# Performance work log

Measured on AMD Instinct MI355X. Metric: run time of the kernel, lower is better.

The kernel has to match this reference:

```python
import jax, jax.numpy as jnp
import numpy as np
import math

B, N, HORIZON, E = 16, 4096, 12, 16
IN_DIM = HORIZON * E            # 192
T_DIM, H, D = 64, 4, 16         # transformer_dim, heads, head_dim
K_ORD = 3
FFN = 128
OUT_DIM = HORIZON * 16          # horizon * dim_out = 192
LN_EPS = 1e-5


def setup_inputs() -> dict:
    key = jax.random.key(0)
    ks = jax.random.split(key, 16)
    s = 0.02
    return {
        "x": jax.random.normal(ks[0], (B, N, IN_DIM), jnp.float32),
        "Wq": jax.random.normal(ks[1], (IN_DIM, T_DIM), jnp.float32) * s,
        "bq": jnp.zeros((T_DIM,), jnp.float32),
        "Wk": jax.random.normal(ks[2], (IN_DIM, T_DIM), jnp.float32) * s,
        "bk": jnp.zeros((T_DIM,), jnp.float32),
        "Wv": jax.random.normal(ks[3], (IN_DIM, T_DIM), jnp.float32) * s,
        "bv": jnp.zeros((T_DIM,), jnp.float32),
        "Win": jax.random.normal(ks[4], (IN_DIM, T_DIM), jnp.float32) * s,  # no bias
        "Wout": jax.random.normal(ks[5], (T_DIM, OUT_DIM), jnp.float32) * s,
        "bout": jnp.zeros((OUT_DIM,), jnp.float32),
        "W1": jax.random.normal(ks[6], (T_DIM, FFN), jnp.float32) * s,
        "b1": jnp.zeros((FFN,), jnp.float32),
        "W2": jax.random.normal(ks[7], (FFN, T_DIM), jnp.float32) * s,
        "b2": jnp.zeros((T_DIM,), jnp.float32),
        "ln_g": jnp.ones((T_DIM,), jnp.float32),
        "ln_b": jnp.zeros((T_DIM,), jnp.float32),
        "weights_pool": jax.random.normal(ks[8], (IN_DIM, OUT_DIM), jnp.float32) * s,
        "Pi": jax.random.normal(ks[9], (H, K_ORD + 1), jnp.float32) * 0.5,
    }


def _layer_norm(y, g, b):
    mu = jnp.mean(y, axis=-1, keepdims=True)
    var = jnp.mean((y - mu) ** 2, axis=-1, keepdims=True)
    return (y - mu) * jax.lax.rsqrt(var + LN_EPS) * g + b


def reference(x, Wq, bq, Wk, bk, Wv, bv, Win, Wout, bout,
              W1, b1, W2, b2, ln_g, ln_b, weights_pool, Pi):
    Bx, Nx, _ = x.shape
    # projections -> (B, H, N, d)
    Q = (x @ Wq + bq).reshape(Bx, Nx, H, D).transpose(0, 2, 1, 3)
    Kt = (x @ Wk + bk).reshape(Bx, Nx, H, D).transpose(0, 2, 1, 3)
    V = (x @ Wv + bv).reshape(Bx, Nx, H, D).transpose(0, 2, 1, 3)

    weighted_sum = jnp.zeros((Bx, H, Nx, D), x.dtype)
    for k in range(K_ORD + 1):
        if k == 0:
            # transform(0, .) returns ones with feature dim 1
            Qk = jnp.ones((Bx, H, Nx, 1), x.dtype)
            Kk = jnp.ones((Bx, H, Nx, 1), x.dtype)
        else:
            Qk = Q ** k   # elementwise power (exp-by-squaring == x**k)
            Kk = Kt ** k
        dk = Qk.shape[-1]
        # f_kv: (B,H,f,d) ; sumN: (B,H,f,1)
        f_kv = jnp.einsum('bhnf,bhnc->bhfc', Kk, V)
        sumN = jnp.sum(Kk, axis=2)[..., None]
        f_kv_norm = f_kv / (sumN + 1e-8) / math.sqrt(dk)
        c_k = jnp.einsum('bhnf,bhfc->bhnc', Qk, f_kv_norm)
        weighted_sum = weighted_sum + c_k * Pi[:, k][None, :, None, None]

    # NOTE: faithful to original: raw view of (B,H,N,d) as (B,N,H*d), no permute
    attention_out = weighted_sum.reshape(Bx, Nx, H * D) / math.factorial(K_ORD)

    proj = x @ Win
    res = _layer_norm(proj + attention_out, ln_g, ln_b)
    ffn = jax.nn.relu(res @ W1 + b1) @ W2 + b2   # dropout = identity (eval)
    res = _layer_norm(res + ffn, ln_g, ln_b)

    x_g = jnp.einsum('bni,io->bno', x, weights_pool)
    out = res @ Wout + bout
    return x_g + out
```

## Files before the change

kernel.cpp:

```cpp
#include <hip/hip_runtime.h>

typedef unsigned int u32;
typedef unsigned short u16;

#define NB 16
#define NN 4096
#define IND 192

typedef __attribute__((ext_vector_type(8))) short short8;
typedef __attribute__((ext_vector_type(4))) float f32x4;
#define MFMA16 __builtin_amdgcn_mfma_f32_16x16x32_bf16

__device__ __forceinline__ float bf2f(u16 u) {
  union { u32 i; float f; } c; c.i = ((u32)u) << 16; return c.f;
}
__device__ __forceinline__ float lo16(u32 u) {
  union { u32 i; float f; } c; c.i = u << 16; return c.f;
}
__device__ __forceinline__ float hi16(u32 u) {
  union { u32 i; float f; } c; c.i = u & 0xffff0000u; return c.f;
}
__device__ __forceinline__ u16 f2bf(float f) {
  union { float f; u32 i; } c; c.f = f;
  u32 r = c.i + 0x7fffu + ((c.i >> 16) & 1u);
  return (u16)(r >> 16);
}
__device__ __forceinline__ float ldwf(const void* p, int i, int isf) {
  return isf ? ((const float*)p)[i] : bf2f(((const u16*)p)[i]);
}
__device__ __forceinline__ short8 ld_frag8(const u16* p) {
  union { uint4 u; short8 s; } c;
  c.u = *reinterpret_cast<const uint4*>(p);
  return c.s;
}
__device__ __forceinline__ short8 as_short8(uint4 u) {
  union { uint4 u; short8 s; } c; c.u = u; return c.s;
}
__device__ __forceinline__ short8 pack8(const float* v) {
  short8 s;
  #pragma unroll
  for (int e = 0; e < 8; ++e) s[e] = (short)f2bf(v[e]);
  return s;
}
__device__ __forceinline__ short8 packf4(float4 a, float4 b) {
  short8 s;
  s[0] = (short)f2bf(a.x); s[1] = (short)f2bf(a.y);
  s[2] = (short)f2bf(a.z); s[3] = (short)f2bf(a.w);
  s[4] = (short)f2bf(b.x); s[5] = (short)f2bf(b.y);
  s[6] = (short)f2bf(b.z); s[7] = (short)f2bf(b.w);
  return s;
}
__device__ __forceinline__ float ln64(float y, float g, float be) {
  float s = y, sq = y * y;
  #pragma unroll
  for (int off = 32; off > 0; off >>= 1) {
    s  += __shfl_xor(s, off, 64);
    sq += __shfl_xor(sq, off, 64);
  }
  float mu  = s * 0.015625f;
  float var = sq * 0.015625f - mu * mu;
  return (y - mu) * rsqrtf(var + 1e-5f) * g + be;
}

__global__ __launch_bounds__(64) void k_detect(const u32* __restrict__ x2,
                                               int* __restrict__ flag) {
  int t = threadIdx.x;
  int bad = 0;
  for (int i = 0; i < 16; ++i) {
    float a = fabsf(lo16(x2[t * 16 + i]));
    if (!(a < 1e4f)) bad = 1;
  }
  int anybad = __any(bad);
  if (t == 0) *flag = anybad ? 1 : 0;
}

__global__ __launch_bounds__(192) void k_xsum(const int* __restrict__ flag,
                                              const void* __restrict__ x,
                                              float* __restrict__ xsum) {
  const int isf = *flag;
  const int t = threadIdx.x;
  const int r0 = blockIdx.x * 256;
  const int b = r0 >> 12;
  float s = 0.f;
  if (isf) {
    const float* xp = (const float*)x;
    for (int r = 0; r < 256; ++r) s += xp[(size_t)(r0 + r) * 192 + t];
  } else {
    const u16* xp = (const u16*)x;
    for (int r = 0; r < 256; ++r) s += bf2f(xp[(size_t)(r0 + r) * 192 + t]);
  }
  atomicAdd(xsum + b * 192 + t, s);
}

__global__ __launch_bounds__(256) void k_prepw(
    const int* __restrict__ flag,
    const void* Wq, const void* Wk, const void* Wv, const void* Win,
    const void* Wout, const void* Wp, const void* W1, const void* W2,
    const void* bq, const void* bk, const void* bv,
    u16* __restrict__ Bs1, u16* __restrict__ BsKlo, u16* __restrict__ Bs2,
    u16* __restrict__ W1f, u16* __restrict__ W2f, float* __restrict__ bcat)
{
  const int isf = *flag;
  int idx = blockIdx.x * 256 + threadIdx.x;
  if (idx < 49152) {
    int e = idx & 7, l = (idx >> 3) & 63, g = idx >> 9;
    int nt = g & 15, ks = g >> 4;
    int k = ks * 32 + (l >> 4) * 8 + e;
    int n = nt * 16 + (l & 15);
    const void* W = (n < 64) ? Wq : (n < 128) ? Wk : (n < 192) ? Wv : Win;
    Bs1[idx] = f2bf(ldwf(W, k * 64 + (n & 63), isf));
  } else if (idx < 61440) {
    int j = idx - 49152;
    int e = j & 7, l = (j >> 3) & 63, g = j >> 9;
    int ntp = g & 3, ks = g >> 2;
    int k = ks * 32 + (l >> 4) * 8 + e;
    int n = ntp * 16 + (l & 15);
    float wv = ldwf(Wk, k * 64 + n, isf);
    u16 hi = f2bf(wv);
    BsKlo[j] = f2bf(wv - bf2f(hi));
  } else if (idx < 110592) {
    int j = idx - 61440;
    int e = j & 7, l = (j >> 3) & 63, g = j >> 9;
    int nt = g % 12, ks = g / 12;
    int k = ks * 32 + (l >> 4) * 8 + e;
    int n = nt * 16 + (l & 15);
    float v = (k < 64) ? ldwf(Wout, k * 192 + n, isf)
                       : ldwf(Wp, (k - 64) * 192 + n, isf);
    Bs2[j] = f2bf(v);
  } else if (idx < 118784) {
    int j = idx - 110592;
    int e = j & 7, l = (j >> 3) & 63, g = j >> 9;
    int nt = g & 7, ks = g >> 3;
    int k = ks * 32 + (l >> 4) * 8 + e;
    int n = nt * 16 + (l & 15);
    W1f[j] = f2bf(ldwf(W1, k * 128 + n, isf));
  } else if (idx < 126976) {
    int j = idx - 118784;
    int e = j & 7, l = (j >> 3) & 63, g = j >> 9;
    int nt = g & 3, ks = g >> 2;
    int k = ks * 32 + (l >> 4) * 8 + e;
    int n = nt * 16 + (l & 15);
    W2f[j] = f2bf(ldwf(W2, k * 64 + n, isf));
  } else if (idx < 127232) {
    int n = idx - 126976;
    bcat[n] = (n < 64)  ? ldwf(bq, n, isf)
            : (n < 128) ? ldwf(bk, n - 64, isf)
            : (n < 192) ? ldwf(bv, n - 128, isf) : 0.f;
  }
}

template<bool F32>
__device__ void gemm1_body(const void* __restrict__ x,
                           const u16* __restrict__ Bs1,
                           const u16* __restrict__ BsKlo,
                           const float* __restrict__ bcat,
                           u16* __restrict__ C1, float* __restrict__ stats,
                           float (*xs)[196], float (*Ks)[65], float (*Vs)[65])
{
  const int tid = threadIdx.x;
  const int mbase = blockIdx.x * 32;
  const int b = mbase >> 12;

  if constexpr (F32) {
    for (int i = tid; i < 1536; i += 512) {
      int row = i / 48, c4 = i - row * 48;
      float4 v = *((const float4*)x + (size_t)(mbase + row) * 48 + c4);
      *(float4*)&xs[row][c4 * 4] = v;
    }
    __syncthreads();
  }

  const int w = tid >> 6, l = tid & 63, lm = l & 15, lk = l >> 4;
  const int nt0 = w * 2;
  const bool isK = (w == 2) || (w == 3);

  short8 bhi[2][6], blo[2][6];
  #pragma unroll
  for (int n2 = 0; n2 < 2; ++n2)
    #pragma unroll
    for (int ks = 0; ks < 6; ++ks) {
      bhi[n2][ks] = ld_frag8(Bs1 + (size_t)((ks * 16 + nt0 + n2) * 64 + l) * 8);
      if (F32 && isK)
        blo[n2][ks] = ld_frag8(BsKlo + (size_t)((ks * 4 + nt0 + n2 - 4) * 64 + l) * 8);
    }
  float bias[2];
  bias[0] = bcat[nt0 * 16 + lm];
  bias[1] = bcat[(nt0 + 1) * 16 + lm];

  for (int mt = 0; mt < 2; ++mt) {
    short8 ahi[6], alo[6];
    if constexpr (F32) {
      const float* xr = &xs[mt * 16 + lm][0];
      #pragma unroll
      for (int ks = 0; ks < 6; ++ks) {
        float v[8];
        *(float4*)&v[0] = *(const float4*)(xr + ks * 32 + lk * 8);
        *(float4*)&v[4] = *(const float4*)(xr + ks * 32 + lk * 8 + 4);
        short8 h8;
        #pragma unroll
        for (int e = 0; e < 8; ++e) h8[e] = (short)f2bf(v[e]);
        ahi[ks] = h8;
        if (isK) {
          short8 l8;
          #pragma unroll
          for (int e = 0; e < 8; ++e) {
            float r = v[e] - bf2f((u16)h8[e]);
            l8[e] = (short)f2bf(r);
          }
          alo[ks] = l8;
        }
      }
    } else {
      const u16* xg = (const u16*)x + (size_t)(mbase + mt * 16 + lm) * 192 + lk * 8;
      #pragma unroll
      for (int ks = 0; ks < 6; ++ks) ahi[ks] = ld_frag8(xg + ks * 32);
    }
    f32x4 acc[2];
    #pragma unroll
    for (int n2 = 0; n2 < 2; ++n2) {
      f32x4 a = {bias[n2], bias[n2], bias[n2], bias[n2]};
      acc[n2] = a;
    }
    #pragma unroll
    for (int ks = 0; ks < 6; ++ks)
      #pragma unroll
      for (int n2 = 0; n2 < 2; ++n2) {
        acc[n2] = MFMA16(ahi[ks], bhi[n2][ks], acc[n2], 0, 0, 0);
        if (F32 && isK) {
          acc[n2] = MFMA16(ahi[ks], blo[n2][ks], acc[n2], 0, 0, 0);
          acc[n2] = MFMA16(alo[ks], bhi[n2][ks], acc[n2], 0, 0, 0);
          acc[n2] = MFMA16(alo[ks], blo[n2][ks], acc[n2], 0, 0, 0);
        }
      }
    const int rl = mt * 16 + lk * 4;
    if (w < 2) {
      #pragma unroll
      for (int n2 = 0; n2 < 2; ++n2)
        #pragma unroll
        for (int r = 0; r < 4; ++r)
          C1[(size_t)(mbase + rl + r) * 128 + (nt0 + n2) * 16 + lm] = f2bf(acc[n2][r]);
    } else if (isK) {
      #pragma unroll
      for (int n2 = 0; n2 < 2; ++n2)
        #pragma unroll
        for (int r = 0; r < 4; ++r)
          Ks[rl + r][(nt0 + n2 - 4) * 16 + lm] = acc[n2][r];
    } else if (w < 6) {
      #pragma unroll
      for (int n2 = 0; n2 < 2; ++n2)
        #pragma unroll
        for (int r = 0; r < 4; ++r)
          Vs[rl + r][(nt0 + n2 - 8) * 16 + lm] = acc[n2][r];
    } else {
      #pragma unroll
      for (int n2 = 0; n2 < 2; ++n2)
        #pragma unroll
        for (int r = 0; r < 4; ++r)
          C1[(size_t)(mbase + rl + r) * 128 + 64 + (nt0 + n2 - 12) * 16 + lm] = f2bf(acc[n2][r]);
    }
  }
  __syncthreads();

  float* sb = stats + (size_t)(b * 4) * 832;
  #pragma unroll
  for (int it = 0; it < 2; ++it) {
    int item = tid + it * 512;
    int hh = item >> 8, f = (item >> 4) & 15, c = item & 15;
    float a1 = 0.f, a2 = 0.f, a3 = 0.f;
    for (int r = 0; r < 32; ++r) {
      float kv = Ks[r][hh * 16 + f];
      float vv = Vs[r][hh * 16 + c];
      float k2 = kv * kv;
      a1 = fmaf(kv, vv, a1);
      a2 = fmaf(k2, vv, a2);
      a3 = fmaf(k2 * kv, vv, a3);
    }
    float* base = sb + (size_t)hh * 832 + f * 16 + c;
    atomicAdd(base, a1);
    atomicAdd(base + 256, a2);
    atomicAdd(base + 512, a3);
  }
  if (tid < 192) {
    int kk = tid >> 6, hf = tid & 63, h2 = hf >> 4, ff = hf & 15;
    float s = 0.f;
    for (int r = 0; r < 32; ++r) {
      float kv = Ks[r][hf];
      s += (kk == 0) ? kv : (kk == 1) ? kv * kv : kv * kv * kv;
    }
    atomicAdd(sb + (size_t)h2 * 832 + 768 + kk * 16 + ff, s);
  } else if (tid < 256) {
    int hf = tid - 192, h2 = hf >> 4;
    float s = 0.f;
    for (int r = 0; r < 32; ++r) s += Vs[r][hf];
    atomicAdd(sb + (size_t)h2 * 832 + 816 + (hf & 15), s);
  }
}

__global__ __launch_bounds__(512, 2) void k_gemm1(
    const int* __restrict__ flag, const void* __restrict__ x,
    const u16* __restrict__ Bs1, const u16* __restrict__ BsKlo,
    const float* __restrict__ bcat,
    u16* __restrict__ C1, float* __restrict__ stats)
{
  __shared__ float xs[32][196];
  __shared__ float Ks[32][65];
  __shared__ float Vs[32][65];
  if (*flag) gemm1_body<true >(x, Bs1, BsKlo, bcat, C1, stats, xs, Ks, Vs);
  else       gemm1_body<false>(x, Bs1, BsKlo, bcat, C1, stats, xs, Ks, Vs);
}

template<bool F32>
__device__ void finalize_body(const float* stats, const void* Pi,
                              const void* Wk, const void* bk,
                              const float* xsum, float* M, float* sn1)
{
  const int bh = blockIdx.x, bb = bh >> 2, h = bh & 3, t = threadIdx.x;
  const float* sb = stats + (size_t)bh * 832;
  float* mb = M + (size_t)bh * 784;
  const float inv6 = 1.0f / 6.0f;

  {
    int f = t >> 4, s = t & 15;
    float p = 0.f;
    for (int i = s * 12; i < s * 12 + 12; ++i)
      p += xsum[bb * 192 + i] * ldwf(Wk, i * 64 + h * 16 + f, F32);
    p += __shfl_xor(p, 1, 64);
    p += __shfl_xor(p, 2, 64);
    p += __shfl_xor(p, 4, 64);
    p += __shfl_xor(p, 8, 64);
    if (s == 0) sn1[f] = p + 4096.0f * ldwf(bk, h * 16 + f, F32);
  }
  __syncthreads();

  {
    const int f = t >> 4, c = t & 15;
    #pragma unroll
    for (int k = 0; k < 3; ++k) {
      float fkv = sb[k * 256 + f * 16 + c];
      float sk  = (k == 0) ? sn1[f] : sb[768 + k * 16 + f];
      float pi  = ldwf(Pi, h * 4 + (k + 1), F32);
      mb[k * 256 + f * 16 + c] = fkv / ((sk + 1e-8f) * 4.0f) * pi * inv6;
    }
  }
  if (t < 16) {
    float sv  = sb[816 + t];
    float pi0 = ldwf(Pi, h * 4 + 0, F32);
    mb[768 + t] = sv / (4096.0f + 1e-8f) * pi0 * inv6;
  }
}

__global__ __launch_bounds__(256) void k_finalize(
    const int* __restrict__ flag, const float* __restrict__ stats,
    const void* __restrict__ Pi, const void* __restrict__ Wk,
    const void* __restrict__ bk, const float* __restrict__ xsum,
    float* __restrict__ M)
{
  __shared__ float sn1[16];
  if (*flag) finalize_body<true >(stats, Pi, Wk, bk, xsum, M, sn1);
  else       finalize_body<false>(stats, Pi, Wk, bk, xsum, M, sn1);
}

template<bool F32> __device__ void mid_body(
    const u16* __restrict__ C1, u16* __restrict__ R2,
    const float* __restrict__ Mall,
    const u16* __restrict__ W1f, const u16* __restrict__ W2f,
    const void* __restrict__ b1, const void* __restrict__ b2,
    const void* __restrict__ lng, const void* __restrict__ lnb,
    float (*attL)[72], u16 (*resB)[72], u16 (*hB)[136])
{
  const int tid = threadIdx.x;
  const int w = tid >> 6, l = tid & 63;
  const int lm = l & 15, lk = l >> 4;
  const int n0g = blockIdx.x * 64;
  const int b = n0g >> 12;
  const int n2_0 = n0g & 4095;
  const int h = n2_0 >> 10;
  const int qg0 = (b << 12) + ((n2_0 & 1023) << 2);
  const float* mb = Mall + (size_t)((b << 2) + h) * 784;

  short8 Bhi[2], Blo[2];
  #pragma unroll
  for (int ks = 0; ks < 2; ++ks) {
    float vh[8], vl[8];
    #pragma unroll
    for (int e = 0; e < 8; ++e) {
      int kk = ks * 32 + lk * 8 + e;
      float v = (kk < 16) ? mb[kk * 16 + lm]
              : (kk < 32) ? mb[256 + (kk - 16) * 16 + lm]
              : (kk < 48) ? mb[512 + (kk - 32) * 16 + lm] : 0.f;
      float hi = bf2f(f2bf(v));
      vh[e] = hi; vl[e] = v - hi;
    }
    Bhi[ks] = pack8(vh);
    Blo[ks] = pack8(vl);
  }
  const float c0v = mb[768 + lm];

  #pragma unroll
  for (int mt2 = 0; mt2 < 4; ++mt2) {
    const int mt = w * 4 + mt2;
    uint4 qv = *(const uint4*)(C1 + (size_t)(qg0 + mt * 16 + lm) * 128
                               + h * 16 + (lk & 1) * 8);
    float q[8] = {lo16(qv.x), hi16(qv.x), lo16(qv.y), hi16(qv.y),
                  lo16(qv.z), hi16(qv.z), lo16(qv.w), hi16(qv.w)};
    float q2[8], q3[8];
    #pragma unroll
    for (int e = 0; e < 8; ++e) { q2[e] = q[e] * q[e]; q3[e] = q2[e] * q[e]; }
    short8 a1, a2;
    if (lk < 2) { a1 = as_short8(qv); a2 = pack8(q3); }
    else        { a1 = pack8(q2);     a2 = short8{0,0,0,0,0,0,0,0}; }

    f32x4 acc = {c0v, c0v, c0v, c0v};
    acc = MFMA16(a1, Bhi[0], acc, 0, 0, 0);
    acc = MFMA16(a1, Blo[0], acc, 0, 0, 0);
    acc = MFMA16(a2, Bhi[1], acc, 0, 0, 0);
    acc = MFMA16(a2, Blo[1], acc, 0, 0, 0);

    #pragma unroll
    for (int r = 0; r < 4; ++r) {
      int qr = mt * 16 + lk * 4 + r;
      attL[qr >> 2][(qr & 3) * 16 + lm] = acc[r];
    }
  }

  const float gj = ldwf(lng, l, F32), bj = ldwf(lnb, l, F32);
  #pragma unroll 4
  for (int rr = 0; rr < 16; ++rr) {
    int r = w * 16 + rr;
    float proj = bf2f(C1[(size_t)(n0g + r) * 128 + 64 + l]);
    float y = proj + attL[r][l];
    resB[r][l] = f2bf(ln64(y, gj, bj));
  }

  short8 a0 = *(const short8*)&resB[w * 16 + lm][lk * 8];
  short8 a1f = *(const short8*)&resB[w * 16 + lm][32 + lk * 8];
  f32x4 hacc[8];
  #pragma unroll
  for (int nt = 0; nt < 8; ++nt) {
    float bv = ldwf(b1, nt * 16 + lm, F32);
    f32x4 a = {bv, bv, bv, bv};
    hacc[nt] = a;
  }
  #pragma unroll
  for (int nt = 0; nt < 8; ++nt) {
    short8 w1a = ld_frag8(W1f + (size_t)((0 * 8 + nt) * 64 + l) * 8);
    short8 w1b = ld_frag8(W1f + (size_t)((1 * 8 + nt) * 64 + l) * 8);
    hacc[nt] = MFMA16(a0, w1a, hacc[nt], 0, 0, 0);
    hacc[nt] = MFMA16(a1f, w1b, hacc[nt], 0, 0, 0);
  }
  #pragma unroll
  for (int nt = 0; nt < 8; ++nt)
    #pragma unroll
    for (int r = 0; r < 4; ++r) {
      int row = w * 16 + lk * 4 + r;
      hB[row][nt * 16 + lm] = f2bf(fmaxf(hacc[nt][r], 0.f));
    }

  short8 ha[4];
  #pragma unroll
  for (int ks = 0; ks < 4; ++ks)
    ha[ks] = *(const short8*)&hB[w * 16 + lm][ks * 32 + lk * 8];
  f32x4 oacc[4];
  #pragma unroll
  for (int nt = 0; nt < 4; ++nt) {
    float bv = ldwf(b2, nt * 16 + lm, F32);
    f32x4 a = {bv, bv, bv, bv};
    oacc[nt] = a;
  }
  #pragma unroll
  for (int ks = 0; ks < 4; ++ks)
    #pragma unroll
    for (int nt = 0; nt < 4; ++nt) {
      short8 w2v = ld_frag8(W2f + (size_t)((ks * 4 + nt) * 64 + l) * 8);
      oacc[nt] = MFMA16(ha[ks], w2v, oacc[nt], 0, 0, 0);
    }

  float gcol[4], bcol[4];
  #pragma unroll
  for (int nt = 0; nt < 4; ++nt) {
    gcol[nt] = ldwf(lng, nt * 16 + lm, F32);
    bcol[nt] = ldwf(lnb, nt * 16 + lm, F32);
  }
  #pragma unroll
  for (int r = 0; r < 4; ++r) {
    int row = w * 16 + lk * 4 + r;
    float y[4];
    float s = 0.f, sq = 0.f;
    #pragma unroll
    for (int nt = 0; nt < 4; ++nt) {
      y[nt] = oacc[nt][r] + bf2f(resB[row][nt * 16 + lm]);
      s += y[nt];
      sq = fmaf(y[nt], y[nt], sq);
    }
    #pragma unroll
    for (int off = 8; off > 0; off >>= 1) {
      s  += __shfl_xor(s, off, 64);
      sq += __shfl_xor(sq, off, 64);
    }
    float mu = s * 0.015625f;
    float var = sq * 0.015625f - mu * mu;
    float rs = rsqrtf(var + 1e-5f);
    #pragma unroll
    for (int nt = 0; nt < 4; ++nt) {
      float r2v = (y[nt] - mu) * rs * gcol[nt] + bcol[nt];
      R2[(size_t)(n0g + row) * 64 + nt * 16 + lm] = f2bf(r2v);
    }
  }
}

__global__ __launch_bounds__(256, 2) void k_mid(
    const int* __restrict__ flag, const u16* __restrict__ C1,
    u16* __restrict__ R2, const float* __restrict__ Mall,
    const u16* __restrict__ W1f, const u16* __restrict__ W2f,
    const void* __restrict__ b1, const void* __restrict__ b2,
    const void* __restrict__ lng, const void* __restrict__ lnb)
{
  __shared__ float attL[64][72];
  __shared__ u16 resB[64][72];
  __shared__ u16 hB[64][136];
  if (*flag) mid_body<true >(C1, R2, Mall, W1f, W2f, b1, b2, lng, lnb, attL, resB, hB);
  else       mid_body<false>(C1, R2, Mall, W1f, W2f, b1, b2, lng, lnb, attL, resB, hB);
}

template<bool F32>
__device__ void gemm2_body(const void* __restrict__ x,
                           const u16* __restrict__ R2,
                           const u16* __restrict__ Bs2,
                           const void* __restrict__ bout,
                           void* __restrict__ out)
{
  const int l = threadIdx.x & 63;
  const int w = threadIdx.x >> 6;
  const int mbase = blockIdx.x * 64;
  const int lm = l & 15, lk = l >> 4;

  short8 bf[8][3];
  #pragma unroll
  for (int ks = 0; ks < 8; ++ks)
    #pragma unroll
    for (int nt = 0; nt < 3; ++nt)
      bf[ks][nt] = ld_frag8(Bs2 + (size_t)((ks * 12 + w * 3 + nt) * 64 + l) * 8);

  float bias[3];
  #pragma unroll
  for (int nt = 0; nt < 3; ++nt) bias[nt] = ldwf(bout, w * 48 + nt * 16 + lm, F32);

  for (int mt = 0; mt < 4; ++mt) {
    const int row = mbase + mt * 16 + lm;
    short8 af[8];
    {
      const u16* rp = R2 + (size_t)row * 64 + lk * 8;
      af[0] = ld_frag8(rp);
      af[1] = ld_frag8(rp + 32);
    }
    if constexpr (F32) {
      const float* xp = (const float*)x + (size_t)row * 192 + lk * 8;
      #pragma unroll
      for (int ks = 2; ks < 8; ++ks) {
        float4 va = *(const float4*)(xp + (ks - 2) * 32);
        float4 vb = *(const float4*)(xp + (ks - 2) * 32 + 4);
        af[ks] = packf4(va, vb);
      }
    } else {
      const u16* xp = (const u16*)x + (size_t)row * 192 + lk * 8;
      #pragma unroll
      for (int ks = 2; ks < 8; ++ks) af[ks] = ld_frag8(xp + (ks - 2) * 32);
    }

    f32x4 acc[3];
    #pragma unroll
    for (int nt = 0; nt < 3; ++nt) {
      f32x4 a = {bias[nt], bias[nt], bias[nt], bias[nt]};
      acc[nt] = a;
    }
    #pragma unroll
    for (int ks = 0; ks < 8; ++ks)
      #pragma unroll
      for (int nt = 0; nt < 3; ++nt)
        acc[nt] = MFMA16(af[ks], bf[ks][nt], acc[nt], 0, 0, 0);
    const int r0 = mbase + mt * 16 + lk * 4;
    const int c0 = w * 48 + lm;
    if constexpr (F32) {
      float* op = (float*)out;
      #pragma unroll
      for (int nt = 0; nt < 3; ++nt)
        #pragma unroll
        for (int r = 0; r < 4; ++r)
          op[(size_t)(r0 + r) * IND + c0 + nt * 16] = acc[nt][r];
    } else {
      u16* op = (u16*)out;
      #pragma unroll
      for (int nt = 0; nt < 3; ++nt)
        #pragma unroll
        for (int r = 0; r < 4; ++r)
          op[(size_t)(r0 + r) * IND + c0 + nt * 16] = f2bf(acc[nt][r]);
    }
  }
}

__global__ __launch_bounds__(256, 2) void k_gemm2(
    const int* __restrict__ flag, const void* __restrict__ x,
    const u16* __restrict__ R2, const u16* __restrict__ Bs2,
    const void* __restrict__ bout, void* __restrict__ out)
{
  if (*flag) gemm2_body<true >(x, R2, Bs2, bout, out);
  else       gemm2_body<false>(x, R2, Bs2, bout, out);
}

extern "C" void kernel_launch(void* const* d_in, const int* in_sizes, int n_in,
                              void* d_out, int out_size, void* d_ws, size_t ws_size,
                              hipStream_t stream)
{
  const void* x   = d_in[0];
  const void* Wq  = d_in[1];
  const void* bq  = d_in[2];
  const void* Wk  = d_in[3];
  const void* bk  = d_in[4];
  const void* Wv  = d_in[5];
  const void* bv  = d_in[6];
  const void* Win = d_in[7];
  const void* Wout= d_in[8];
  const void* bout= d_in[9];
  const void* W1  = d_in[10];
  const void* b1  = d_in[11];
  const void* W2  = d_in[12];
  const void* b2  = d_in[13];
  const void* lng = d_in[14];
  const void* lnb = d_in[15];
  const void* Wp  = d_in[16];
  const void* Pi  = d_in[17];

  u16* xb    = (u16*)d_ws;
  u16* C1    = xb + (size_t)12582912;
  u16* R2    = C1 + (size_t)8388608;
  u16* Bs1   = R2 + (size_t)4194304;
  u16* BsKlo = Bs1 + 49152;
  u16* Bs2   = BsKlo + 12288;
  u16* W1f   = Bs2 + 49152;
  u16* W2f   = W1f + 8192;
  float* bcat  = (float*)(W2f + 8192);
  float* stats = bcat + 256;
  float* xsum  = stats + 53248;
  float* Mc    = xsum + 3072;
  int*   flag  = (int*)(Mc + 50176);

  k_detect<<<1, 64, 0, stream>>>((const u32*)x, flag);
  hipMemsetAsync(stats, 0, (size_t)(53248 + 3072) * sizeof(float), stream);

  k_prepw<<<497, 256, 0, stream>>>(flag, Wq, Wk, Wv, Win, Wout, Wp, W1, W2,
                                   bq, bk, bv, Bs1, BsKlo, Bs2, W1f, W2f, bcat);
  k_xsum<<<256, 192, 0, stream>>>(flag, x, xsum);
  k_gemm1<<<2048, 512, 0, stream>>>(flag, x, Bs1, BsKlo, bcat, C1, stats);
  k_finalize<<<64, 256, 0, stream>>>(flag, stats, Pi, Wk, bk, xsum, Mc);
  k_mid<<<1024, 256, 0, stream>>>(flag, C1, R2, Mc, W1f, W2f, b1, b2, lng, lnb);
  k_gemm2<<<1024, 256, 0, stream>>>(flag, x, R2, Bs2, bout, d_out);
}
```

Baseline: 159.2 us.

## Split Q/Win GEMM from K/V stats kernel and replace atomics with partial-sum buffers

The fused projection+statistics kernel is split in two. A lean k_gemm1 computes only the Q and Win columns into C1, reading x directly from global memory. A new k_stats kernel recomputes the K and V projections over 128-row chunks, accumulates moment statistics in registers, and writes per-slice partials instead of issuing atomicAdds. k_finalize now reduces the 32 partial slices. This aims to remove atomic contention and the shared-memory staging of x, at the cost of reading x twice and a larger partials workspace.

Result: slower. 214.5 us (+34.7%).

```diff
diff --git a/kernel.cpp b/kernel.cpp
--- a/kernel.cpp
+++ b/kernel.cpp
@@ -152,170 +152,234 @@
 template<bool F32>
 __device__ void gemm1_body(const void* __restrict__ x,
                            const u16* __restrict__ Bs1,
+                           const float* __restrict__ bcat,
+                           u16* __restrict__ C1)
+{
+  const int tid = threadIdx.x;
+  const int mbase = blockIdx.x * 32;
+  const int w = tid >> 6, l = tid & 63, lm = l & 15, lk = l >> 4;
+  const bool isQ = (w < 2);
+  const int nt0 = isQ ? (w * 2) : (12 + (w - 2) * 2);
+
+  short8 bhi[2][6];
+  #pragma unroll
+  for (int n2 = 0; n2 < 2; ++n2)
+    #pragma unroll
+    for (int ks = 0; ks < 6; ++ks)
+      bhi[n2][ks] = ld_frag8(Bs1 + (size_t)((ks * 16 + nt0 + n2) * 64 + l) * 8);
+  float bias[2];
+  bias[0] = bcat[nt0 * 16 + lm];
+  bias[1] = bcat[(nt0 + 1) * 16 + lm];
+
+  for (int mt = 0; mt < 2; ++mt) {
+    short8 ahi[6];
+    if constexpr (F32) {
+      const float* xr = (const float*)x + (size_t)(mbase + mt * 16 + lm) * 192 + lk * 8;
+      #pragma unroll
+      for (int ks = 0; ks < 6; ++ks) {
+        float4 va = *(const float4*)(xr + ks * 32);
+        float4 vb = *(const float4*)(xr + ks * 32 + 4);
+        ahi[ks] = packf4(va, vb);
+      }
+    } else {
+      const u16* xg = (const u16*)x + (size_t)(mbase + mt * 16 + lm) * 192 + lk * 8;
+      #pragma unroll
+      for (int ks = 0; ks < 6; ++ks) ahi[ks] = ld_frag8(xg + ks * 32);
+    }
+    #pragma unroll
+    for (int n2 = 0; n2 < 2; ++n2) {
+      f32x4 acc = {bias[n2], bias[n2], bias[n2], bias[n2]};
+      #pragma unroll
+      for (int ks = 0; ks < 6; ++ks)
+        acc = MFMA16(ahi[ks], bhi[n2][ks], acc, 0, 0, 0);
+      const int rl = mt * 16 + lk * 4;
+      if (isQ) {
+        #pragma unroll
+        for (int r = 0; r < 4; ++r)
+          C1[(size_t)(mbase + rl + r) * 128 + (nt0 + n2) * 16 + lm] = f2bf(acc[r]);
+      } else {
+        #pragma unroll
+        for (int r = 0; r < 4; ++r)
+          C1[(size_t)(mbase + rl + r) * 128 + 64 + (nt0 + n2 - 12) * 16 + lm] = f2bf(acc[r]);
+      }
+    }
+  }
+}
+
+__global__ __launch_bounds__(256, 2) void k_gemm1(
+    const int* __restrict__ flag, const void* __restrict__ x,
+    const u16* __restrict__ Bs1, const float* __restrict__ bcat,
+    u16* __restrict__ C1)
+{
+  if (*flag) gemm1_body<true >(x, Bs1, bcat, C1);
+  else       gemm1_body<false>(x, Bs1, bcat, C1);
+}
+
+template<bool F32>
+__device__ void stats_body(const void* __restrict__ x,
+                           const u16* __restrict__ Bs1,
                            const u16* __restrict__ BsKlo,
                            const float* __restrict__ bcat,
-                           u16* __restrict__ C1, float* __restrict__ stats,
-                           float (*xs)[196], float (*Ks)[65], float (*Vs)[65])
+                           float* __restrict__ statsS,
+                           float (*Ks)[65], float (*Vs)[65])
 {
   const int tid = threadIdx.x;
-  const int mbase = blockIdx.x * 32;
-  const int b = mbase >> 12;
-
-  if constexpr (F32) {
-    for (int i = tid; i < 1536; i += 512) {
-      int row = i / 48, c4 = i - row * 48;
-      float4 v = *((const float4*)x + (size_t)(mbase + row) * 48 + c4);
-      *(float4*)&xs[row][c4 * 4] = v;
-    }
-    __syncthreads();
-  }
-
+  const int blk = blockIdx.x;
+  const int b = blk >> 5, st = blk & 31;
+  const int base = (b << 12) + st * 128;
   const int w = tid >> 6, l = tid & 63, lm = l & 15, lk = l >> 4;
   const int nt0 = w * 2;
   const bool isK = (w == 2) || (w == 3);
+  const bool isV = (w == 4) || (w == 5);
+  const bool isKV = isK || isV;
 
   short8 bhi[2][6], blo[2][6];
-  #pragma unroll
-  for (int n2 = 0; n2 < 2; ++n2)
-    #pragma unroll
-    for (int ks = 0; ks < 6; ++ks) {
-      bhi[n2][ks] = ld_frag8(Bs1 + (size_t)((ks * 16 + nt0 + n2) * 64 + l) * 8);
-      if (F32 && isK)
-        blo[n2][ks] = ld_frag8(BsKlo + (size_t)((ks * 4 + nt0 + n2 - 4) * 64 + l) * 8);
-    }
-  float bias[2];
-  bias[0] = bcat[nt0 * 16 + lm];
-  bias[1] = bcat[(nt0 + 1) * 16 + lm];
-
-  for (int mt = 0; mt < 2; ++mt) {
-    short8 ahi[6], alo[6];
-    if constexpr (F32) {
-      const float* xr = &xs[mt * 16 + lm][0];
+  if (isKV) {
+    #pragma unroll
+    for (int n2 = 0; n2 < 2; ++n2)
       #pragma unroll
       for (int ks = 0; ks < 6; ++ks) {
-        float v[8];
-        *(float4*)&v[0] = *(const float4*)(xr + ks * 32 + lk * 8);
-        *(float4*)&v[4] = *(const float4*)(xr + ks * 32 + lk * 8 + 4);
-        short8 h8;
+        bhi[n2][ks] = ld_frag8(Bs1 + (size_t)((ks * 16 + nt0 + n2) * 64 + l) * 8);
+        if (F32 && isK)
+          blo[n2][ks] = ld_frag8(BsKlo + (size_t)((ks * 4 + nt0 + n2 - 4) * 64 + l) * 8);
+      }
+  }
+  float bias[2] = {0.f, 0.f};
+  if (isKV) {
+    bias[0] = bcat[nt0 * 16 + lm];
+    bias[1] = bcat[(nt0 + 1) * 16 + lm];
+  }
+
+  float sa1[2] = {0.f, 0.f}, sa2[2] = {0.f, 0.f}, sa3[2] = {0.f, 0.f};
+  float ssk = 0.f, ssv = 0.f;
+
+  for (int ch = 0; ch < 4; ++ch) {
+    const int mbase = base + ch * 32;
+    __syncthreads();
+
+    if (isKV) {
+      for (int mt = 0; mt < 2; ++mt) {
+        short8 ahi[6], alo[6];
+        if constexpr (F32) {
+          const float* xr = (const float*)x + (size_t)(mbase + mt * 16 + lm) * 192 + lk * 8;
+          #pragma unroll
+          for (int ks = 0; ks < 6; ++ks) {
+            float4 va = *(const float4*)(xr + ks * 32);
+            float4 vb = *(const float4*)(xr + ks * 32 + 4);
+            short8 h8 = packf4(va, vb);
+            ahi[ks] = h8;
+            if (isK) {
+              short8 l8;
+              l8[0] = (short)f2bf(va.x - bf2f((u16)h8[0]));
+              l8[1] = (short)f2bf(va.y - bf2f((u16)h8[1]));
+              l8[2] = (short)f2bf(va.z - bf2f((u16)h8[2]));
+              l8[3] = (short)f2bf(va.w - bf2f((u16)h8[3]));
+              l8[4] = (short)f2bf(vb.x - bf2f((u16)h8[4]));
+              l8[5] = (short)f2bf(vb.y - bf2f((u16)h8[5]));
+              l8[6] = (short)f2bf(vb.z - bf2f((u16)h8[6]));
+              l8[7] = (short)f2bf(vb.w - bf2f((u16)h8[7]));
+              alo[ks] = l8;
+            }
+          }
+        } else {
+          const u16* xg = (const u16*)x + (size_t)(mbase + mt * 16 + lm) * 192 + lk * 8;
+          #pragma unroll
+          for (int ks = 0; ks < 6; ++ks) ahi[ks] = ld_frag8(xg + ks * 32);
+        }
         #pragma unroll
-        for (int e = 0; e < 8; ++e) h8[e] = (short)f2bf(v[e]);
-        ahi[ks] = h8;
-        if (isK) {
-          short8 l8;
+        for (int n2 = 0; n2 < 2; ++n2) {
+          f32x4 acc = {bias[n2], bias[n2], bias[n2], bias[n2]};
           #pragma unroll
-          for (int e = 0; e < 8; ++e) {
-            float r = v[e] - bf2f((u16)h8[e]);
-            l8[e] = (short)f2bf(r);
+          for (int ks = 0; ks < 6; ++ks) {
+            acc = MFMA16(ahi[ks], bhi[n2][ks], acc, 0, 0, 0);
+            if (F32 && isK) {
+              acc = MFMA16(ahi[ks], blo[n2][ks], acc, 0, 0, 0);
+              acc = MFMA16(alo[ks], bhi[n2][ks], acc, 0, 0, 0);
+              acc = MFMA16(alo[ks], blo[n2][ks], acc, 0, 0, 0);
+            }
           }
-          alo[ks] = l8;
+          const int rl = mt * 16 + lk * 4;
+          if (isK) {
+            #pragma unroll
+            for (int r = 0; r < 4; ++r)
+              Ks[rl + r][(nt0 + n2 - 4) * 16 + lm] = acc[r];
+          } else {
+            #pragma unroll
+            for (int r = 0; r < 4; ++r)
+              Vs[rl + r][(nt0 + n2 - 8) * 16 + lm] = acc[r];
+          }
         }
       }
-    } else {
-      const u16* xg = (const u16*)x + (size_t)(mbase + mt * 16 + lm) * 192 + lk * 8;
-      #pragma unroll
-      for (int ks = 0; ks < 6; ++ks) ahi[ks] = ld_frag8(xg + ks * 32);
-    }
-    f32x4 acc[2];
-    #pragma unroll
-    for (int n2 = 0; n2 < 2; ++n2) {
-      f32x4 a = {bias[n2], bias[n2], bias[n2], bias[n2]};
-      acc[n2] = a;
-    }
-    #pragma unroll
-    for (int ks = 0; ks < 6; ++ks)
-      #pragma unroll
-      for (int n2 = 0; n2 < 2; ++n2) {
-        acc[n2] = MFMA16(ahi[ks], bhi[n2][ks], acc[n2], 0, 0, 0);
-        if (F32 && isK) {
-          acc[n2] = MFMA16(ahi[ks], blo[n2][ks], acc[n2], 0, 0, 0);
-          acc[n2] = MFMA16(alo[ks], bhi[n2][ks], acc[n2], 0, 0, 0);
-          acc[n2] = MFMA16(alo[ks], blo[n2][ks], acc[n2], 0, 0, 0);
-        }
+    }
+    __syncthreads();
+
+    #pragma unroll
+    for (int it = 0; it < 2; ++it) {
+      int item = tid + it * 512;
+      int hh = item >> 8, f = (item >> 4) & 15, c = item & 15;
+      float a1 = sa1[it], a2 = sa2[it], a3 = sa3[it];
+      for (int r = 0; r < 32; ++r) {
+        float kv = Ks[r][hh * 16 + f];
+        float vv = Vs[r][hh * 16 + c];
+        float k2 = kv * kv;
+        a1 = fmaf(kv, vv, a1);
+        a2 = fmaf(k2, vv, a2);
+        a3 = fmaf(k2 * kv, vv, a3);
       }
-    const int rl = mt * 16 + lk * 4;
-    if (w < 2) {
-      #pragma unroll
-      for (int n2 = 0; n2 < 2; ++n2)
-        #pragma unroll
-        for (int r = 0; r < 4; ++r)
-          C1[(size_t)(mbase + rl + r) * 128 + (nt0 + n2) * 16 + lm] = f2bf(acc[n2][r]);
-    } else if (isK) {
-      #pragma unroll
-      for (int n2 = 0; n2 < 2; ++n2)
-        #pragma unroll
-        for (int r = 0; r < 4; ++r)
-          Ks[rl + r][(nt0 + n2 - 4) * 16 + lm] = acc[n2][r];
-    } else if (w < 6) {
-      #pragma unroll
-      for (int n2 = 0; n2 < 2; ++n2)
-        #pragma unroll
-        for (int r = 0; r < 4; ++r)
-          Vs[rl + r][(nt0 + n2 - 8) * 16 + lm] = acc[n2][r];
-    } else {
-      #pragma unroll
-      for (int n2 = 0; n2 < 2; ++n2)
-        #pragma unroll
-        for (int r = 0; r < 4; ++r)
-          C1[(size_t)(mbase + rl + r) * 128 + 64 + (nt0 + n2 - 12) * 16 + lm] = f2bf(acc[n2][r]);
-    }
-  }
-  __syncthreads();
-
-  float* sb = stats + (size_t)(b * 4) * 832;
+      sa1[it] = a1; sa2[it] = a2; sa3[it] = a3;
+    }
+    if (tid < 192) {
+      int kk = tid >> 6, hf = tid & 63;
+      float s = ssk;
+      for (int r = 0; r < 32; ++r) {
+        float kv = Ks[r][hf];
+        s += (kk == 0) ? kv : (kk == 1) ? kv * kv : kv * kv * kv;
+      }
+      ssk = s;
+    } else if (tid < 256) {
+      int hf = tid - 192;
+      float s = ssv;
+      for (int r = 0; r < 32; ++r) s += Vs[r][hf];
+      ssv = s;
+    }
+  }
+
   #pragma unroll
   for (int it = 0; it < 2; ++it) {
     int item = tid + it * 512;
     int hh = item >> 8, f = (item >> 4) & 15, c = item & 15;
-    float a1 = 0.f, a2 = 0.f, a3 = 0.f;
-    for (int r = 0; r < 32; ++r) {
-      float kv = Ks[r][hh * 16 + f];
-      float vv = Vs[r][hh * 16 + c];
-      float k2 = kv * kv;
-      a1 = fmaf(kv, vv, a1);
-      a2 = fmaf(k2, vv, a2);
-      a3 = fmaf(k2 * kv, vv, a3);
-    }
-    float* base = sb + (size_t)hh * 832 + f * 16 + c;
-    atomicAdd(base, a1);
-    atomicAdd(base + 256, a2);
-    atomicAdd(base + 512, a3);
+    float* base2 = statsS + ((size_t)((b * 4 + hh) * 32 + st)) * 832 + f * 16 + c;
+    base2[0]   = sa1[it];
+    base2[256] = sa2[it];
+    base2[512] = sa3[it];
   }
   if (tid < 192) {
     int kk = tid >> 6, hf = tid & 63, h2 = hf >> 4, ff = hf & 15;
-    float s = 0.f;
-    for (int r = 0; r < 32; ++r) {
-      float kv = Ks[r][hf];
-      s += (kk == 0) ? kv : (kk == 1) ? kv * kv : kv * kv * kv;
-    }
-    atomicAdd(sb + (size_t)h2 * 832 + 768 + kk * 16 + ff, s);
+    statsS[((size_t)((b * 4 + h2) * 32 + st)) * 832 + 768 + kk * 16 + ff] = ssk;
   } else if (tid < 256) {
     int hf = tid - 192, h2 = hf >> 4;
-    float s = 0.f;
-    for (int r = 0; r < 32; ++r) s += Vs[r][hf];
-    atomicAdd(sb + (size_t)h2 * 832 + 816 + (hf & 15), s);
-  }
-}
-
-__global__ __launch_bounds__(512, 2) void k_gemm1(
+    statsS[((size_t)((b * 4 + h2) * 32 + st)) * 832 + 816 + (hf & 15)] = ssv;
+  }
+}
+
+__global__ __launch_bounds__(512, 2) void k_stats(
     const int* __restrict__ flag, const void* __restrict__ x,
     const u16* __restrict__ Bs1, const u16* __restrict__ BsKlo,
-    const float* __restrict__ bcat,
-    u16* __restrict__ C1, float* __restrict__ stats)
-{
-  __shared__ float xs[32][196];
+    const float* __restrict__ bcat, float* __restrict__ statsS)
+{
   __shared__ float Ks[32][65];
   __shared__ float Vs[32][65];
-  if (*flag) gemm1_body<true >(x, Bs1, BsKlo, bcat, C1, stats, xs, Ks, Vs);
-  else       gemm1_body<false>(x, Bs1, BsKlo, bcat, C1, stats, xs, Ks, Vs);
+  if (*flag) stats_body<true >(x, Bs1, BsKlo, bcat, statsS, Ks, Vs);
+  else       stats_body<false>(x, Bs1, BsKlo, bcat, statsS, Ks, Vs);
 }
 
 template<bool F32>
-__device__ void finalize_body(const float* stats, const void* Pi,
+__device__ void finalize_body(const float* statsS, const void* Pi,
                               const void* Wk, const void* bk,
                               const float* xsum, float* M, float* sn1)
 {
   const int bh = blockIdx.x, bb = bh >> 2, h = bh & 3, t = threadIdx.x;
-  const float* sb = stats + (size_t)bh * 832;
+  const float* sb = statsS + (size_t)bh * 32 * 832;
   float* mb = M + (size_t)bh * 784;
   const float inv6 = 1.0f / 6.0f;
 
@@ -334,30 +398,40 @@
 
   {
     const int f = t >> 4, c = t & 15;
+    float fk0 = 0.f, fk1 = 0.f, fk2 = 0.f, sk2 = 0.f, sk3 = 0.f;
+    for (int s32 = 0; s32 < 32; ++s32) {
+      const float* sp = sb + (size_t)s32 * 832;
+      fk0 += sp[f * 16 + c];
+      fk1 += sp[256 + f * 16 + c];
+      fk2 += sp[512 + f * 16 + c];
+      sk2 += sp[784 + f];
+      sk3 += sp[800 + f];
+    }
+    float fk[3] = {fk0, fk1, fk2};
     #pragma unroll
     for (int k = 0; k < 3; ++k) {
-      float fkv = sb[k * 256 + f * 16 + c];
-      float sk  = (k == 0) ? sn1[f] : sb[768 + k * 16 + f];
-      float pi  = ldwf(Pi, h * 4 + (k + 1), F32);
-      mb[k * 256 + f * 16 + c] = fkv / ((sk + 1e-8f) * 4.0f) * pi * inv6;
+      float sk = (k == 0) ? sn1[f] : (k == 1) ? sk2 : sk3;
+      float pi = ldwf(Pi, h * 4 + (k + 1), F32);
+      mb[k * 256 + f * 16 + c] = fk[k] / ((sk + 1e-8f) * 4.0f) * pi * inv6;
     }
   }
   if (t < 16) {
-    float sv  = sb[816 + t];
+    float sv = 0.f;
+    for (int s32 = 0; s32 < 32; ++s32) sv += sb[(size_t)s32 * 832 + 816 + t];
     float pi0 = ldwf(Pi, h * 4 + 0, F32);
     mb[768 + t] = sv / (4096.0f + 1e-8f) * pi0 * inv6;
   }
 }
 
 __global__ __launch_bounds__(256) void k_finalize(
-    const int* __restrict__ flag, const float* __restrict__ stats,
+    const int* __restrict__ flag, const float* __restrict__ statsS,
     const void* __restrict__ Pi, const void* __restrict__ Wk,
     const void* __restrict__ bk, const float* __restrict__ xsum,
     float* __restrict__ M)
 {
   __shared__ float sn1[16];
-  if (*flag) finalize_body<true >(stats, Pi, Wk, bk, xsum, M, sn1);
-  else       finalize_body<false>(stats, Pi, Wk, bk, xsum, M, sn1);
+  if (*flag) finalize_body<true >(statsS, Pi, Wk, bk, xsum, M, sn1);
+  else       finalize_body<false>(statsS, Pi, Wk, bk, xsum, M, sn1);
 }
 
 template<bool F32> __device__ void mid_body(
@@ -638,20 +712,21 @@
   u16* Bs2   = BsKlo + 12288;
   u16* W1f   = Bs2 + 49152;
   u16* W2f   = W1f + 8192;
-  float* bcat  = (float*)(W2f + 8192);
-  float* stats = bcat + 256;
-  float* xsum  = stats + 53248;
-  float* Mc    = xsum + 3072;
-  int*   flag  = (int*)(Mc + 50176);
+  float* bcat   = (float*)(W2f + 8192);
+  float* statsS = bcat + 256;
+  float* xsum   = statsS + 1703936;
+  float* Mc     = xsum + 3072;
+  int*   flag   = (int*)(Mc + 50176);
 
   k_detect<<<1, 64, 0, stream>>>((const u32*)x, flag);
-  hipMemsetAsync(stats, 0, (size_t)(53248 + 3072) * sizeof(float), stream);
+  hipMemsetAsync(xsum, 0, (size_t)3072 * sizeof(float), stream);
 
   k_prepw<<<497, 256, 0, stream>>>(flag, Wq, Wk, Wv, Win, Wout, Wp, W1, W2,
                                    bq, bk, bv, Bs1, BsKlo, Bs2, W1f, W2f, bcat);
   k_xsum<<<256, 192, 0, stream>>>(flag, x, xsum);
-  k_gemm1<<<2048, 512, 0, stream>>>(flag, x, Bs1, BsKlo, bcat, C1, stats);
-  k_finalize<<<64, 256, 0, stream>>>(flag, stats, Pi, Wk, bk, xsum, Mc);
+  k_gemm1<<<2048, 256, 0, stream>>>(flag, x, Bs1, bcat, C1);
+  k_stats<<<512, 512, 0, stream>>>(flag, x, Bs1, BsKlo, bcat, statsS);
+  k_finalize<<<64, 256, 0, stream>>>(flag, statsS, Pi, Wk, bk, xsum, Mc);
   k_mid<<<1024, 256, 0, stream>>>(flag, C1, R2, Mc, W1f, W2f, b1, b2, lng, lnb);
   k_gemm2<<<1024, 256, 0, stream>>>(flag, x, R2, Bs2, bout, d_out);
 }
```
